# Kernel optimization log

Measured on AMD Instinct MI355X. Metric: run time of the kernel, lower is better.

The kernel has to match this reference:

```python
import jax, jax.numpy as jnp
import numpy as np

B, S, D, H = 4, 1024, 1024, 16
DH = D // H


def _ln(x, g, b, eps=1e-5):
    m = x.mean(-1, keepdims=True)
    v = ((x - m) ** 2).mean(-1, keepdims=True)
    return (x - m) / jnp.sqrt(v + eps) * g + b


def setup_inputs() -> dict:
    key = jax.random.key(0)
    ks = jax.random.split(key, 8)
    s = 0.02
    return {
        "x": jax.random.normal(ks[0], (B, S, D), jnp.float32),
        # attention projections (bias=False). Stored as [in, out] = torch W.T
        "Wq": jax.random.normal(ks[1], (D, D), jnp.float32) * s,
        "Wk": jax.random.normal(ks[2], (D, D), jnp.float32) * s,
        "Wv": jax.random.normal(ks[3], (D, D), jnp.float32) * s,
        # LayerNorms: ln_start, ln_add_left, ln_add_right, ln_ff
        "g0": jnp.ones((D,), jnp.float32), "b0": jnp.zeros((D,), jnp.float32),
        "gl": jnp.ones((D,), jnp.float32), "bl": jnp.zeros((D,), jnp.float32),
        "gr": jnp.ones((D,), jnp.float32), "br": jnp.zeros((D,), jnp.float32),
        "gf": jnp.ones((D,), jnp.float32), "bf": jnp.zeros((D,), jnp.float32),
        # FF: fc1, fc2 are dim_H -> dim_H with bias
        "W1": jax.random.normal(ks[4], (D, D), jnp.float32) * s,
        "b1": jnp.zeros((D,), jnp.float32),
        "W2": jax.random.normal(ks[5], (D, D), jnp.float32) * s,
        "b2": jnp.zeros((D,), jnp.float32),
    }


def _block(x, Wq, Wk, Wv, g0, b0, gl, bl, gr, br, gf, bf, W1, b1, W2, b2):
    b, s, d = x.shape
    # --- ResiDual MHA ---
    x_ln = _ln(x, g0, b0)
    q = (x_ln @ Wq).reshape(b, s, H, DH)
    k = (x_ln @ Wk).reshape(b, s, H, DH)
    v = (x_ln @ Wv).reshape(b, s, H, DH)
    scores = jnp.einsum("bqhd,bkhd->bhqk", q, k) / np.sqrt(DH).astype(np.float32)
    attn = jax.nn.softmax(scores, axis=-1)
    o = jnp.einsum("bhqk,bkhd->bqhd", attn, v).reshape(b, s, d)
    # note: fc_o is defined in the module but never applied in forward
    left = _ln(x_ln + o, gl, bl)   # ln_add_left
    right = _ln(x + o, gr, br)     # ln_add_right (original residual)
    y = left + right
    # --- FF (pre_ln=False -> ln is Identity), erf GELU ---
    h = y @ W1 + b1
    h = h * 0.5 * (1.0 + jax.lax.erf(h / np.sqrt(2.0).astype(np.float32)))
    y = y + (h @ W2 + b2)
    # --- ln_ff ---
    return _ln(y, gf, bf)


def reference(x, Wq, Wk, Wv, g0, b0, gl, bl, gr, br, gf, bf, W1, b1, W2, b2):
    return _block(x, Wq, Wk, Wv, g0, b0, gl, bl, gr, br, gf, bf, W1, b1, W2, b2)
```

## Files before the change

kernel.cpp:

```cpp
#include <hip/hip_runtime.h>
#include <hip/hip_bf16.h>

typedef __attribute__((ext_vector_type(8))) short bf16x8;
typedef __attribute__((ext_vector_type(4))) float f32x4;
typedef __attribute__((ext_vector_type(4))) short s16x4;

#define DEV static __device__ __forceinline__

DEV short f2bf(float f) {
    unsigned u = __builtin_bit_cast(unsigned, f);
    unsigned r = (u + 0x7fffu + ((u >> 16) & 1u)) >> 16;
    return (short)r;
}

DEV float bf2f(short s) {
    return __builtin_bit_cast(float, ((unsigned)(unsigned short)s) << 16);
}

DEV unsigned pk_bf16(float lo, float hi) {
    __hip_bfloat162 h = __float22bfloat162_rn(make_float2(lo, hi));
    unsigned u;
    __builtin_memcpy(&u, &h, 4);
    return u;
}

DEV void gl_lds16(const void* g, void* l) {
    __builtin_amdgcn_global_load_lds(
        (const __attribute__((address_space(1))) unsigned*)g,
        (__attribute__((address_space(3))) unsigned*)l, 16, 0, 0);
}

DEV float wave_sum(float v) {
    #pragma unroll
    for (int off = 32; off; off >>= 1) v += __shfl_down(v, off, 64);
    return v;
}

DEV float block_sum(float v, float* sm, int t) {
    v = wave_sum(v);
    if ((t & 63) == 0) sm[t >> 6] = v;
    __syncthreads();
    float r = sm[0] + sm[1] + sm[2] + sm[3];
    __syncthreads();
    return r;
}

__global__ __launch_bounds__(256) void transpose_all(
    const float* __restrict__ Wq, const float* __restrict__ Wk,
    const float* __restrict__ Wv, const float* __restrict__ W1,
    const float* __restrict__ W2, short* __restrict__ wqkvT,
    short* __restrict__ w1T, short* __restrict__ w2T, float qscale) {
    __shared__ float tile[32][33];
    const int z = blockIdx.z;
    const float* W;
    short* out;
    float scale = 1.f;
    if (z == 0)      { W = Wq; out = wqkvT;           scale = qscale; }
    else if (z == 1) { W = Wk; out = wqkvT + 1048576; }
    else if (z == 2) { W = Wv; out = wqkvT + 2097152; }
    else if (z == 3) { W = W1; out = w1T; }
    else             { W = W2; out = w2T; }
    int t = threadIdx.x;
    int tx = t & 31, ty = t >> 5;
    int bx = blockIdx.x, by = blockIdx.y;
    #pragma unroll
    for (int i = 0; i < 4; i++) {
        int k = by * 32 + ty + i * 8;
        tile[ty + i * 8][tx] = W[(size_t)k * 1024 + bx * 32 + tx];
    }
    __syncthreads();
    #pragma unroll
    for (int i = 0; i < 4; i++) {
        int n = bx * 32 + ty + i * 8;
        int k = by * 32 + tx;
        out[(size_t)n * 1024 + k] = f2bf(tile[tx][ty + i * 8] * scale);
    }
}

__global__ __launch_bounds__(256) void ln0_kernel(const float* __restrict__ x,
                                                  const float* __restrict__ g,
                                                  const float* __restrict__ b,
                                                  short* __restrict__ xbf) {
    __shared__ float sm[4];
    int row = blockIdx.x, t = threadIdx.x;
    const f32x4 v = *(const f32x4*)(x + (size_t)row * 1024 + t * 4);
    float mean = block_sum(v[0] + v[1] + v[2] + v[3], sm, t) * 0.0009765625f;
    f32x4 d;
    float sq = 0.f;
    #pragma unroll
    for (int j = 0; j < 4; j++) { d[j] = v[j] - mean; sq += d[j] * d[j]; }
    float var = block_sum(sq, sm, t) * 0.0009765625f;
    float inv = rsqrtf(var + 1e-5f);
    const f32x4 gv = *(const f32x4*)(g + t * 4);
    const f32x4 bv = *(const f32x4*)(b + t * 4);
    s16x4 ob;
    #pragma unroll
    for (int j = 0; j < 4; j++) ob[j] = f2bf(d[j] * inv * gv[j] + bv[j]);
    *(s16x4*)(xbf + (size_t)row * 1024 + t * 4) = ob;
}

__global__ __launch_bounds__(256) void ln_dual_kernel(
    const float* __restrict__ x, const short* __restrict__ xln,
    const short* __restrict__ o, const float* __restrict__ gl,
    const float* __restrict__ bl, const float* __restrict__ gr,
    const float* __restrict__ br, short* __restrict__ ybf) {
    __shared__ float sm[4];
    int row = blockIdx.x, t = threadIdx.x;
    size_t base = (size_t)row * 1024 + t * 4;
    const f32x4 xv = *(const f32x4*)(x + base);
    const s16x4 xl = *(const s16x4*)(xln + base);
    const s16x4 ob = *(const s16x4*)(o + base);
    f32x4 u, w;
    #pragma unroll
    for (int j = 0; j < 4; j++) {
        float ov = bf2f(ob[j]);
        u[j] = bf2f(xl[j]) + ov; w[j] = xv[j] + ov;
    }
    float mu = block_sum(u[0] + u[1] + u[2] + u[3], sm, t) * 0.0009765625f;
    float mw = block_sum(w[0] + w[1] + w[2] + w[3], sm, t) * 0.0009765625f;
    float squ = 0.f, sqw = 0.f;
    #pragma unroll
    for (int j = 0; j < 4; j++) {
        u[j] -= mu; squ += u[j] * u[j];
        w[j] -= mw; sqw += w[j] * w[j];
    }
    float iu = rsqrtf(block_sum(squ, sm, t) * 0.0009765625f + 1e-5f);
    float iw = rsqrtf(block_sum(sqw, sm, t) * 0.0009765625f + 1e-5f);
    const f32x4 glv = *(const f32x4*)(gl + t * 4);
    const f32x4 blv = *(const f32x4*)(bl + t * 4);
    const f32x4 grv = *(const f32x4*)(gr + t * 4);
    const f32x4 brv = *(const f32x4*)(br + t * 4);
    s16x4 yb;
    #pragma unroll
    for (int j = 0; j < 4; j++)
        yb[j] = f2bf(u[j] * iu * glv[j] + blv[j] + w[j] * iw * grv[j] + brv[j]);
    *(s16x4*)(ybf + base) = yb;
}

__global__ __launch_bounds__(256) void ln_final_kernel(const short* __restrict__ z,
                                                       const float* __restrict__ g,
                                                       const float* __restrict__ b,
                                                       float* __restrict__ out) {
    __shared__ float sm[4];
    int row = blockIdx.x, t = threadIdx.x;
    const s16x4 zv = *(const s16x4*)(z + (size_t)row * 1024 + t * 4);
    f32x4 v;
    #pragma unroll
    for (int j = 0; j < 4; j++) v[j] = bf2f(zv[j]);
    float mean = block_sum(v[0] + v[1] + v[2] + v[3], sm, t) * 0.0009765625f;
    f32x4 d;
    float sq = 0.f;
    #pragma unroll
    for (int j = 0; j < 4; j++) { d[j] = v[j] - mean; sq += d[j] * d[j]; }
    float var = block_sum(sq, sm, t) * 0.0009765625f;
    float inv = rsqrtf(var + 1e-5f);
    const f32x4 gv = *(const f32x4*)(g + t * 4);
    const f32x4 bv = *(const f32x4*)(b + t * 4);
    f32x4 o;
    #pragma unroll
    for (int j = 0; j < 4; j++) o[j] = d[j] * inv * gv[j] + bv[j];
    *(f32x4*)(out + (size_t)row * 1024 + t * 4) = o;
}

template <int MODE, int BN>
__global__ __launch_bounds__(256, 3) void gemm_bt(
    const short* __restrict__ A, const short* __restrict__ Bt,
    short* __restrict__ outq, short* __restrict__ outk, short* __restrict__ outvt,
    const float* __restrict__ bias, short* __restrict__ outbf,
    const short* __restrict__ yresid, short* __restrict__ outz) {
    constexpr int NF = BN / 32;
    __shared__ short SH[128 * 64 + BN * 64];
    short* As = SH;
    short* Bs = SH + 128 * 64;
    const int t = threadIdx.x;
    const int lane = t & 63;
    const int w = t >> 6;
    const int wr = w >> 1, wc = w & 1;
    const int l16 = lane & 15, lhi = lane >> 4;
    const int m0 = blockIdx.x * 128;
    const int n0 = blockIdx.y * BN;

    f32x4 acc[4][NF] = {};

    for (int kt = 0; kt < 1024; kt += 64) {
        __syncthreads();
        #pragma unroll
        for (int i = 0; i < 4; i++) {
            int tt = i * 256 + t;
            int row = tt >> 3, c = tt & 7;
            int sw = ((c ^ (row & 7)) << 4);
            gl_lds16((const char*)A + ((size_t)(m0 + row) * 1024 + kt) * 2 + sw,
                     (char*)As + i * 4096 + w * 1024);
        }
        #pragma unroll
        for (int i = 0; i < BN / 32; i++) {
            int tt = i * 256 + t;
            int row = tt >> 3, c = tt & 7;
            int sw = ((c ^ (row & 7)) << 4);
            gl_lds16((const char*)Bt + ((size_t)(n0 + row) * 1024 + kt) * 2 + sw,
                     (char*)Bs + i * 4096 + w * 1024);
        }
        __syncthreads();
        #pragma unroll
        for (int ks = 0; ks < 2; ks++) {
            bf16x8 af[4], bfr[NF];
            #pragma unroll
            for (int mi = 0; mi < 4; mi++) {
                int row = wr * 64 + mi * 16 + l16;
                int c = (ks * 4 + lhi) ^ (row & 7);
                af[mi] = *(const bf16x8*)((const char*)As + row * 128 + c * 16);
            }
            #pragma unroll
            for (int ni = 0; ni < NF; ni++) {
                int row = wc * (BN / 2) + ni * 16 + l16;
                int c = (ks * 4 + lhi) ^ (row & 7);
                bfr[ni] = *(const bf16x8*)((const char*)Bs + row * 128 + c * 16);
            }
            #pragma unroll
            for (int mi = 0; mi < 4; mi++)
                #pragma unroll
                for (int ni = 0; ni < NF; ni++)
                    acc[mi][ni] = __builtin_amdgcn_mfma_f32_16x16x32_bf16(
                        af[mi], bfr[ni], acc[mi][ni], 0, 0, 0);
        }
    }

    if (MODE == 0 && n0 >= 2048) {
        __syncthreads();
        #pragma unroll
        for (int mi = 0; mi < 4; mi++) {
            #pragma unroll
            for (int ni = 0; ni < NF; ni++) {
                int m0l = wr * 64 + mi * 16 + lhi * 4;
                int n_l = wc * 64 + ni * 16 + l16;
                s16x4 pk;
                #pragma unroll
                for (int r = 0; r < 4; r++) pk[r] = f2bf(acc[mi][ni][r]);
                int byte = n_l * 256 + ((m0l * 2) ^ ((n_l & 7) << 4));
                *(s16x4*)((char*)SH + byte) = pk;
            }
        }
        __syncthreads();
        const int b = m0 >> 10;
        const int srow0 = m0 & 1023;
        #pragma unroll
        for (int it = 0; it < 8; it++) {
            int n_l = it * 16 + w * 4 + lhi;
            int chunk = l16;
            int byte = n_l * 256 + ((chunk * 16) ^ ((n_l & 7) << 4));
            bf16x8 vv = *(const bf16x8*)((const char*)SH + byte);
            int nn = n0 - 2048 + n_l;
            int hh = nn >> 6, dh = nn & 63;
            int bh = b * 16 + hh;
            *(bf16x8*)(outvt + ((size_t)bh * 64 + dh) * 1024 + srow0 + chunk * 8) = vv;
        }
        return;
    }

    #pragma unroll
    for (int mi = 0; mi < 4; mi++) {
        #pragma unroll
        for (int ni = 0; ni < NF; ni++) {
            #pragma unroll
            for (int r = 0; r < 4; r++) {
                int m = m0 + wr * 64 + mi * 16 + lhi * 4 + r;
                int n = n0 + wc * (BN / 2) + ni * 16 + l16;
                float vacc = acc[mi][ni][r];
                if (MODE == 0) {
                    int which = n >> 10, nn = n & 1023;
                    int h = nn >> 6, dh = nn & 63;
                    int b = m >> 10, s = m & 1023;
                    int bh = b * 16 + h;
                    if (which == 0)
                        outq[((size_t)bh * 1024 + s) * 64 + dh] = f2bf(vacc);
                    else
                        outk[((size_t)bh * 1024 + s) * 64 + dh] = f2bf(vacc);
                } else if (MODE == 1) {
                    float hv = vacc + bias[n];
                    float ge = hv * 0.5f * (1.f + erff(hv * 0.70710678118654752f));
                    outbf[(size_t)m * 1024 + n] = f2bf(ge);
                } else {
                    float zz = vacc + bias[n] + bf2f(yresid[(size_t)m * 1024 + n]);
                    outz[(size_t)m * 1024 + n] = f2bf(zz);
                }
            }
        }
    }
}

__global__ __launch_bounds__(512, 4) void attn_kernel(
    const short* __restrict__ qb, const short* __restrict__ kb,
    const short* __restrict__ vtb, short* __restrict__ obuf) {
    __shared__ short Ks[2 * 128 * 64];
    __shared__ short Vs[2 * 64 * 128];
    __shared__ short Ps[8 * 16 * 64];

    const int t = threadIdx.x, lane = t & 63, w = t >> 6;
    const int l16 = lane & 15, lhi = lane >> 4;
    const int blk = blockIdx.x;
    const int qt = (blk >> 3) & 7;
    const int bh = (blk & 7) * 8 + (blk >> 6);
    const short* kp = kb + (size_t)bh * 65536;
    const short* vp = vtb + (size_t)bh * 65536;

    const short* qp = qb + (size_t)bh * 65536 + (size_t)(qt * 128 + w * 16 + l16) * 64;
    bf16x8 qfr[2];
    qfr[0] = *(const bf16x8*)(qp + lhi * 8);
    qfr[1] = *(const bf16x8*)(qp + 32 + lhi * 8);

    f32x4 o[4] = {};
    float lrun = 0.f;

    const int krow = t >> 3;
    const int ksw = (((t & 7) ^ (krow & 7)) << 4);
    const int vrow = t >> 4;
    const int vsw = (((t & 15) ^ (vrow & 7)) << 4);

    #pragma unroll
    for (int i = 0; i < 2; i++) {
        gl_lds16((const char*)kp + (size_t)(i * 64 + krow) * 128 + ksw,
                 (char*)Ks + i * 8192 + w * 1024);
        gl_lds16((const char*)vp + (size_t)(i * 32 + vrow) * 2048 + vsw,
                 (char*)Vs + i * 8192 + w * 1024);
    }

    short* pw = Ps + w * 1024;
    int cur = 0;

    for (int kv = 0; kv < 8; kv++) {
        asm volatile("s_waitcnt vmcnt(0)");
        __syncthreads();
        if (kv < 7) {
            int nb = cur ^ 1;
            #pragma unroll
            for (int i = 0; i < 2; i++) {
                gl_lds16((const char*)kp +
                             (size_t)((kv + 1) * 128 + i * 64 + krow) * 128 + ksw,
                         (char*)Ks + nb * 16384 + i * 8192 + w * 1024);
                gl_lds16((const char*)vp + (size_t)(i * 32 + vrow) * 2048 +
                             (kv + 1) * 256 + vsw,
                         (char*)Vs + nb * 16384 + i * 8192 + w * 1024);
            }
        }
        const char* kbase = (const char*)Ks + cur * 16384;
        const char* vbase = (const char*)Vs + cur * 16384;

        #pragma unroll
        for (int sub = 0; sub < 2; sub++) {
            f32x4 sc[4];
            __builtin_amdgcn_s_setprio(1);
            #pragma unroll
            for (int kvb = 0; kvb < 4; kvb++) {
                f32x4 s4 = {};
                #pragma unroll
                for (int c = 0; c < 2; c++) {
                    int row = sub * 64 + kvb * 16 + l16;
                    int cc = (c * 4 + lhi) ^ (row & 7);
                    bf16x8 kf = *(const bf16x8*)(kbase + row * 128 + cc * 16);
                    s4 = __builtin_amdgcn_mfma_f32_16x16x32_bf16(kf, qfr[c], s4, 0, 0, 0);
                }
                sc[kvb] = s4;
            }
            __builtin_amdgcn_s_setprio(0);

            float rs = 0.f;
            #pragma unroll
            for (int kvb = 0; kvb < 4; kvb++) {
                #pragma unroll
                for (int r = 0; r < 4; r++) {
                    float p = __builtin_amdgcn_exp2f(sc[kvb][r]);
                    sc[kvb][r] = p;
                    rs += p;
                }
            }
            rs += __shfl_xor(rs, 16, 64);
            rs += __shfl_xor(rs, 32, 64);
            lrun += rs;

            #pragma unroll
            for (int kvb = 0; kvb < 4; kvb++) {
                uint2 pk;
                pk.x = pk_bf16(sc[kvb][0], sc[kvb][1]);
                pk.y = pk_bf16(sc[kvb][2], sc[kvb][3]);
                int bytecol = kvb * 32 + lhi * 8;
                int addr = l16 * 128 + ((((bytecol >> 4) ^ (l16 & 7)) << 4)) + (bytecol & 15);
                *(uint2*)((char*)pw + addr) = pk;
            }

            bf16x8 pa[2];
            #pragma unroll
            for (int c = 0; c < 2; c++) {
                int cc = (c * 4 + lhi) ^ (l16 & 7);
                pa[c] = *(const bf16x8*)((const char*)pw + l16 * 128 + cc * 16);
            }
            __builtin_amdgcn_s_setprio(1);
            #pragma unroll
            for (int d = 0; d < 4; d++) {
                #pragma unroll
                for (int c = 0; c < 2; c++) {
                    int vr = d * 16 + l16;
                    int sbyte = (sub * 128 + c * 64 + lhi * 16) ^ ((vr & 7) << 4);
                    bf16x8 vf = *(const bf16x8*)(vbase + vr * 256 + sbyte);
                    o[d] = __builtin_amdgcn_mfma_f32_16x16x32_bf16(vf, pa[c], o[d], 0, 0, 0);
                }
            }
            __builtin_amdgcn_s_setprio(0);
        }
        cur ^= 1;
    }

    const int b = bh >> 4, h = bh & 15;
    const int s = qt * 128 + w * 16 + l16;
    float linv = 1.0f / lrun;
    #pragma unroll
    for (int d = 0; d < 4; d++) {
        s16x4 ov;
        #pragma unroll
        for (int r = 0; r < 4; r++) ov[r] = f2bf(o[d][r] * linv);
        *(s16x4*)(obuf + ((size_t)(b * 1024 + s)) * 1024 + h * 64 + d * 16 + lhi * 4) = ov;
    }
}

extern "C" void kernel_launch(void* const* d_in, const int* in_sizes, int n_in,
                              void* d_out, int out_size, void* d_ws, size_t ws_size,
                              hipStream_t stream) {
    const float* x  = (const float*)d_in[0];
    const float* Wq = (const float*)d_in[1];
    const float* Wk = (const float*)d_in[2];
    const float* Wv = (const float*)d_in[3];
    const float* g0 = (const float*)d_in[4];
    const float* b0 = (const float*)d_in[5];
    const float* gl = (const float*)d_in[6];
    const float* bl = (const float*)d_in[7];
    const float* gr = (const float*)d_in[8];
    const float* br = (const float*)d_in[9];
    const float* gf = (const float*)d_in[10];
    const float* bfp = (const float*)d_in[11];
    const float* W1 = (const float*)d_in[12];
    const float* b1 = (const float*)d_in[13];
    const float* W2 = (const float*)d_in[14];
    const float* b2 = (const float*)d_in[15];

    char* ws = (char*)d_ws;
    short* xlnbf = (short*)(ws);
    short* wqkvT = (short*)(ws + ((size_t)8 << 20));
    short* w1T   = (short*)(ws + ((size_t)14 << 20));
    short* w2T   = (short*)(ws + ((size_t)16 << 20));
    short* qb    = (short*)(ws + ((size_t)18 << 20));
    short* kb    = (short*)(ws + ((size_t)26 << 20));
    short* vtb   = (short*)(ws + ((size_t)34 << 20));
    short* obuf  = (short*)(ws + ((size_t)42 << 20));
    short* ybf   = (short*)(ws + ((size_t)50 << 20));
    short* hbf   = (short*)(ws + ((size_t)58 << 20));
    short* zbf   = (short*)(ws + ((size_t)66 << 20));

    dim3 b256(256);
    transpose_all<<<dim3(32, 32, 5), b256, 0, stream>>>(Wq, Wk, Wv, W1, W2,
                                                        wqkvT, w1T, w2T,
                                                        0.180336880f);

    ln0_kernel<<<4096, b256, 0, stream>>>(x, g0, b0, xlnbf);

    gemm_bt<0, 128><<<dim3(32, 24), b256, 0, stream>>>(
        xlnbf, wqkvT, qb, kb, vtb, nullptr, nullptr, nullptr, nullptr);

    attn_kernel<<<512, dim3(512), 0, stream>>>(qb, kb, vtb, obuf);

    ln_dual_kernel<<<4096, b256, 0, stream>>>(x, xlnbf, obuf, gl, bl, gr, br, ybf);

    gemm_bt<1, 64><<<dim3(32, 16), b256, 0, stream>>>(
        ybf, w1T, nullptr, nullptr, nullptr, b1, hbf, nullptr, nullptr);

    gemm_bt<2, 64><<<dim3(32, 16), b256, 0, stream>>>(
        hbf, w2T, nullptr, nullptr, nullptr, b2, nullptr, ybf, zbf);

    ln_final_kernel<<<4096, b256, 0, stream>>>(zbf, gf, bfp, (float*)d_out);
}
```

Baseline: 129.0 us.

## Merge weight transpose with LN0 and give each attention wave two query tiles

```diff
diff --git a/kernel.cpp b/kernel.cpp
--- a/kernel.cpp
+++ b/kernel.cpp
@@ -45,58 +45,57 @@
     return r;
 }
 
-__global__ __launch_bounds__(256) void transpose_all(
+__global__ __launch_bounds__(256) void wprep_kernel(
     const float* __restrict__ Wq, const float* __restrict__ Wk,
     const float* __restrict__ Wv, const float* __restrict__ W1,
     const float* __restrict__ W2, short* __restrict__ wqkvT,
-    short* __restrict__ w1T, short* __restrict__ w2T, float qscale) {
+    short* __restrict__ w1T, short* __restrict__ w2T,
+    const float* __restrict__ x, const float* __restrict__ g0,
+    const float* __restrict__ b0, short* __restrict__ xbf, float qscale) {
     __shared__ float tile[32][33];
     const int z = blockIdx.z;
-    const float* W;
-    short* out;
-    float scale = 1.f;
-    if (z == 0)      { W = Wq; out = wqkvT;           scale = qscale; }
-    else if (z == 1) { W = Wk; out = wqkvT + 1048576; }
-    else if (z == 2) { W = Wv; out = wqkvT + 2097152; }
-    else if (z == 3) { W = W1; out = w1T; }
-    else             { W = W2; out = w2T; }
-    int t = threadIdx.x;
-    int tx = t & 31, ty = t >> 5;
-    int bx = blockIdx.x, by = blockIdx.y;
-    #pragma unroll
-    for (int i = 0; i < 4; i++) {
-        int k = by * 32 + ty + i * 8;
-        tile[ty + i * 8][tx] = W[(size_t)k * 1024 + bx * 32 + tx];
-    }
-    __syncthreads();
-    #pragma unroll
-    for (int i = 0; i < 4; i++) {
-        int n = bx * 32 + ty + i * 8;
-        int k = by * 32 + tx;
-        out[(size_t)n * 1024 + k] = f2bf(tile[tx][ty + i * 8] * scale);
-    }
-}
-
-__global__ __launch_bounds__(256) void ln0_kernel(const float* __restrict__ x,
-                                                  const float* __restrict__ g,
-                                                  const float* __restrict__ b,
-                                                  short* __restrict__ xbf) {
-    __shared__ float sm[4];
-    int row = blockIdx.x, t = threadIdx.x;
-    const f32x4 v = *(const f32x4*)(x + (size_t)row * 1024 + t * 4);
-    float mean = block_sum(v[0] + v[1] + v[2] + v[3], sm, t) * 0.0009765625f;
-    f32x4 d;
-    float sq = 0.f;
-    #pragma unroll
-    for (int j = 0; j < 4; j++) { d[j] = v[j] - mean; sq += d[j] * d[j]; }
-    float var = block_sum(sq, sm, t) * 0.0009765625f;
-    float inv = rsqrtf(var + 1e-5f);
-    const f32x4 gv = *(const f32x4*)(g + t * 4);
-    const f32x4 bv = *(const f32x4*)(b + t * 4);
-    s16x4 ob;
-    #pragma unroll
-    for (int j = 0; j < 4; j++) ob[j] = f2bf(d[j] * inv * gv[j] + bv[j]);
-    *(s16x4*)(xbf + (size_t)row * 1024 + t * 4) = ob;
+    const int t = threadIdx.x;
+    if (z < 5) {
+        const float* W;
+        short* out;
+        float scale = 1.f;
+        if (z == 0)      { W = Wq; out = wqkvT;           scale = qscale; }
+        else if (z == 1) { W = Wk; out = wqkvT + 1048576; }
+        else if (z == 2) { W = Wv; out = wqkvT + 2097152; }
+        else if (z == 3) { W = W1; out = w1T; }
+        else             { W = W2; out = w2T; }
+        int tx = t & 31, ty = t >> 5;
+        int bx = blockIdx.x, by = blockIdx.y;
+        #pragma unroll
+        for (int i = 0; i < 4; i++) {
+            int k = by * 32 + ty + i * 8;
+            tile[ty + i * 8][tx] = W[(size_t)k * 1024 + bx * 32 + tx];
+        }
+        __syncthreads();
+        #pragma unroll
+        for (int i = 0; i < 4; i++) {
+            int n = bx * 32 + ty + i * 8;
+            int k = by * 32 + tx;
+            out[(size_t)n * 1024 + k] = f2bf(tile[tx][ty + i * 8] * scale);
+        }
+    } else {
+        float* sm = &tile[0][0];
+        int row = (z - 5) * 1024 + blockIdx.y * 32 + blockIdx.x;
+        const f32x4 v = *(const f32x4*)(x + (size_t)row * 1024 + t * 4);
+        float mean = block_sum(v[0] + v[1] + v[2] + v[3], sm, t) * 0.0009765625f;
+        f32x4 d;
+        float sq = 0.f;
+        #pragma unroll
+        for (int j = 0; j < 4; j++) { d[j] = v[j] - mean; sq += d[j] * d[j]; }
+        float var = block_sum(sq, sm, t) * 0.0009765625f;
+        float inv = rsqrtf(var + 1e-5f);
+        const f32x4 gv = *(const f32x4*)(g0 + t * 4);
+        const f32x4 bv = *(const f32x4*)(b0 + t * 4);
+        s16x4 ob;
+        #pragma unroll
+        for (int j = 0; j < 4; j++) ob[j] = f2bf(d[j] * inv * gv[j] + bv[j]);
+        *(s16x4*)(xbf + (size_t)row * 1024 + t * 4) = ob;
+    }
 }
 
 __global__ __launch_bounds__(256) void ln_dual_kernel(
@@ -288,12 +287,12 @@
     }
 }
 
-__global__ __launch_bounds__(512, 4) void attn_kernel(
+__global__ __launch_bounds__(256, 2) void attn_kernel(
     const short* __restrict__ qb, const short* __restrict__ kb,
     const short* __restrict__ vtb, short* __restrict__ obuf) {
     __shared__ short Ks[2 * 128 * 64];
     __shared__ short Vs[2 * 64 * 128];
-    __shared__ short Ps[8 * 16 * 64];
+    __shared__ short Ps[4 * 2 * 16 * 64];
 
     const int t = threadIdx.x, lane = t & 63, w = t >> 6;
     const int l16 = lane & 15, lhi = lane >> 4;
@@ -303,28 +302,32 @@
     const short* kp = kb + (size_t)bh * 65536;
     const short* vp = vtb + (size_t)bh * 65536;
 
-    const short* qp = qb + (size_t)bh * 65536 + (size_t)(qt * 128 + w * 16 + l16) * 64;
-    bf16x8 qfr[2];
-    qfr[0] = *(const bf16x8*)(qp + lhi * 8);
-    qfr[1] = *(const bf16x8*)(qp + 32 + lhi * 8);
-
-    f32x4 o[4] = {};
-    float lrun = 0.f;
-
-    const int krow = t >> 3;
-    const int ksw = (((t & 7) ^ (krow & 7)) << 4);
-    const int vrow = t >> 4;
-    const int vsw = (((t & 15) ^ (vrow & 7)) << 4);
-
-    #pragma unroll
-    for (int i = 0; i < 2; i++) {
-        gl_lds16((const char*)kp + (size_t)(i * 64 + krow) * 128 + ksw,
-                 (char*)Ks + i * 8192 + w * 1024);
-        gl_lds16((const char*)vp + (size_t)(i * 32 + vrow) * 2048 + vsw,
-                 (char*)Vs + i * 8192 + w * 1024);
-    }
-
-    short* pw = Ps + w * 1024;
+    const short* qp0 = qb + (size_t)bh * 65536 +
+                       (size_t)(qt * 128 + w * 32 + l16) * 64;
+    bf16x8 qfr[2][2];
+    qfr[0][0] = *(const bf16x8*)(qp0 + lhi * 8);
+    qfr[0][1] = *(const bf16x8*)(qp0 + 32 + lhi * 8);
+    qfr[1][0] = *(const bf16x8*)(qp0 + 1024 + lhi * 8);
+    qfr[1][1] = *(const bf16x8*)(qp0 + 1024 + 32 + lhi * 8);
+
+    f32x4 o0[4] = {}, o1[4] = {};
+    float lr0 = 0.f, lr1 = 0.f;
+
+    const int kr = t >> 3, kc = t & 7;
+    const int vr8 = t >> 4, vc = t & 15;
+
+    #pragma unroll
+    for (int i = 0; i < 4; i++) {
+        int krow = i * 32 + kr;
+        gl_lds16((const char*)kp + (size_t)krow * 128 + ((kc ^ (krow & 7)) << 4),
+                 (char*)Ks + i * 4096 + w * 1024);
+        int vrow = i * 16 + vr8;
+        gl_lds16((const char*)vp + (size_t)vrow * 2048 + ((vc ^ (vrow & 7)) << 4),
+                 (char*)Vs + i * 4096 + w * 1024);
+    }
+
+    char* pw0 = (char*)Ps + w * 4096;
+    char* pw1 = pw0 + 2048;
     int cur = 0;
 
     for (int kv = 0; kv < 8; kv++) {
@@ -333,13 +336,16 @@
         if (kv < 7) {
             int nb = cur ^ 1;
             #pragma unroll
-            for (int i = 0; i < 2; i++) {
+            for (int i = 0; i < 4; i++) {
+                int krow = i * 32 + kr;
                 gl_lds16((const char*)kp +
-                             (size_t)((kv + 1) * 128 + i * 64 + krow) * 128 + ksw,
-                         (char*)Ks + nb * 16384 + i * 8192 + w * 1024);
-                gl_lds16((const char*)vp + (size_t)(i * 32 + vrow) * 2048 +
-                             (kv + 1) * 256 + vsw,
-                         (char*)Vs + nb * 16384 + i * 8192 + w * 1024);
+                             (size_t)((kv + 1) * 128 + krow) * 128 +
+                             ((kc ^ (krow & 7)) << 4),
+                         (char*)Ks + nb * 16384 + i * 4096 + w * 1024);
+                int vrow = i * 16 + vr8;
+                gl_lds16((const char*)vp + (size_t)vrow * 2048 + (kv + 1) * 256 +
+                             ((vc ^ (vrow & 7)) << 4),
+                         (char*)Vs + nb * 16384 + i * 4096 + w * 1024);
             }
         }
         const char* kbase = (const char*)Ks + cur * 16384;
@@ -347,51 +353,60 @@
 
         #pragma unroll
         for (int sub = 0; sub < 2; sub++) {
-            f32x4 sc[4];
+            f32x4 s0[4], s1[4];
+            #pragma unroll
+            for (int kvb = 0; kvb < 4; kvb++) { s0[kvb] = f32x4{}; s1[kvb] = f32x4{}; }
             __builtin_amdgcn_s_setprio(1);
             #pragma unroll
             for (int kvb = 0; kvb < 4; kvb++) {
-                f32x4 s4 = {};
                 #pragma unroll
                 for (int c = 0; c < 2; c++) {
                     int row = sub * 64 + kvb * 16 + l16;
                     int cc = (c * 4 + lhi) ^ (row & 7);
                     bf16x8 kf = *(const bf16x8*)(kbase + row * 128 + cc * 16);
-                    s4 = __builtin_amdgcn_mfma_f32_16x16x32_bf16(kf, qfr[c], s4, 0, 0, 0);
+                    s0[kvb] = __builtin_amdgcn_mfma_f32_16x16x32_bf16(
+                        kf, qfr[0][c], s0[kvb], 0, 0, 0);
+                    s1[kvb] = __builtin_amdgcn_mfma_f32_16x16x32_bf16(
+                        kf, qfr[1][c], s1[kvb], 0, 0, 0);
                 }
-                sc[kvb] = s4;
             }
             __builtin_amdgcn_s_setprio(0);
 
-            float rs = 0.f;
+            float rs0 = 0.f, rs1 = 0.f;
             #pragma unroll
             for (int kvb = 0; kvb < 4; kvb++) {
                 #pragma unroll
                 for (int r = 0; r < 4; r++) {
-                    float p = __builtin_amdgcn_exp2f(sc[kvb][r]);
-                    sc[kvb][r] = p;
-                    rs += p;
+                    float p0 = __builtin_amdgcn_exp2f(s0[kvb][r]);
+                    float p1 = __builtin_amdgcn_exp2f(s1[kvb][r]);
+                    s0[kvb][r] = p0; rs0 += p0;
+                    s1[kvb][r] = p1; rs1 += p1;
                 }
             }
-            rs += __shfl_xor(rs, 16, 64);
-            rs += __shfl_xor(rs, 32, 64);
-            lrun += rs;
+            rs0 += __shfl_xor(rs0, 16, 64); rs0 += __shfl_xor(rs0, 32, 64);
+            rs1 += __shfl_xor(rs1, 16, 64); rs1 += __shfl_xor(rs1, 32, 64);
+            lr0 += rs0; lr1 += rs1;
 
             #pragma unroll
             for (int kvb = 0; kvb < 4; kvb++) {
+                int bytecol = kvb * 32 + lhi * 8;
+                int addr = l16 * 128 + ((((bytecol >> 4) ^ (l16 & 7)) << 4)) +
+                           (bytecol & 15);
                 uint2 pk;
-                pk.x = pk_bf16(sc[kvb][0], sc[kvb][1]);
-                pk.y = pk_bf16(sc[kvb][2], sc[kvb][3]);
-                int bytecol = kvb * 32 + lhi * 8;
-                int addr = l16 * 128 + ((((bytecol >> 4) ^ (l16 & 7)) << 4)) + (bytecol & 15);
-                *(uint2*)((char*)pw + addr) = pk;
-            }
-
-            bf16x8 pa[2];
+                pk.x = pk_bf16(s0[kvb][0], s0[kvb][1]);
+                pk.y = pk_bf16(s0[kvb][2], s0[kvb][3]);
+                *(uint2*)(pw0 + addr) = pk;
+                pk.x = pk_bf16(s1[kvb][0], s1[kvb][1]);
+                pk.y = pk_bf16(s1[kvb][2], s1[kvb][3]);
+                *(uint2*)(pw1 + addr) = pk;
+            }
+
+            bf16x8 pa0[2], pa1[2];
             #pragma unroll
             for (int c = 0; c < 2; c++) {
                 int cc = (c * 4 + lhi) ^ (l16 & 7);
-                pa[c] = *(const bf16x8*)((const char*)pw + l16 * 128 + cc * 16);
+                pa0[c] = *(const bf16x8*)(pw0 + l16 * 128 + cc * 16);
+                pa1[c] = *(const bf16x8*)(pw1 + l16 * 128 + cc * 16);
             }
             __builtin_amdgcn_s_setprio(1);
             #pragma unroll
@@ -401,7 +416,10 @@
                     int vr = d * 16 + l16;
                     int sbyte = (sub * 128 + c * 64 + lhi * 16) ^ ((vr & 7) << 4);
                     bf16x8 vf = *(const bf16x8*)(vbase + vr * 256 + sbyte);
-                    o[d] = __builtin_amdgcn_mfma_f32_16x16x32_bf16(vf, pa[c], o[d], 0, 0, 0);
+                    o0[d] = __builtin_amdgcn_mfma_f32_16x16x32_bf16(
+                        vf, pa0[c], o0[d], 0, 0, 0);
+                    o1[d] = __builtin_amdgcn_mfma_f32_16x16x32_bf16(
+                        vf, pa1[c], o1[d], 0, 0, 0);
                 }
             }
             __builtin_amdgcn_s_setprio(0);
@@ -410,14 +428,19 @@
     }
 
     const int b = bh >> 4, h = bh & 15;
-    const int s = qt * 128 + w * 16 + l16;
-    float linv = 1.0f / lrun;
+    const int srow0 = qt * 128 + w * 32 + l16;
+    float li0 = 1.0f / lr0, li1 = 1.0f / lr1;
     #pragma unroll
     for (int d = 0; d < 4; d++) {
         s16x4 ov;
         #pragma unroll
-        for (int r = 0; r < 4; r++) ov[r] = f2bf(o[d][r] * linv);
-        *(s16x4*)(obuf + ((size_t)(b * 1024 + s)) * 1024 + h * 64 + d * 16 + lhi * 4) = ov;
+        for (int r = 0; r < 4; r++) ov[r] = f2bf(o0[d][r] * li0);
+        *(s16x4*)(obuf + ((size_t)(b * 1024 + srow0)) * 1024 + h * 64 + d * 16 +
+                  lhi * 4) = ov;
+        #pragma unroll
+        for (int r = 0; r < 4; r++) ov[r] = f2bf(o1[d][r] * li1);
+        *(s16x4*)(obuf + ((size_t)(b * 1024 + srow0 + 16)) * 1024 + h * 64 +
+                  d * 16 + lhi * 4) = ov;
     }
 }
 
@@ -455,16 +478,13 @@
     short* zbf   = (short*)(ws + ((size_t)66 << 20));
 
     dim3 b256(256);
-    transpose_all<<<dim3(32, 32, 5), b256, 0, stream>>>(Wq, Wk, Wv, W1, W2,
-                                                        wqkvT, w1T, w2T,
-                                                        0.180336880f);
-
-    ln0_kernel<<<4096, b256, 0, stream>>>(x, g0, b0, xlnbf);
+    wprep_kernel<<<dim3(32, 32, 9), b256, 0, stream>>>(
+        Wq, Wk, Wv, W1, W2, wqkvT, w1T, w2T, x, g0, b0, xlnbf, 0.180336880f);
 
     gemm_bt<0, 128><<<dim3(32, 24), b256, 0, stream>>>(
         xlnbf, wqkvT, qb, kb, vtb, nullptr, nullptr, nullptr, nullptr);
 
-    attn_kernel<<<512, dim3(512), 0, stream>>>(qb, kb, vtb, obuf);
+    attn_kernel<<<512, b256, 0, stream>>>(qb, kb, vtb, obuf);
 
     ln_dual_kernel<<<4096, b256, 0, stream>>>(x, xlnbf, obuf, gl, bl, gr, br, ybf);
 
```

Result: no change. 127.2 us (-1.5%).
